# Kernel optimization log

Measured on AMD Instinct MI355X. Metric: run time of the kernel, lower is better.

Reference implementation:

```python
import jax, jax.numpy as jnp
import numpy as np

EPS = 1e-5

def _temporal_conv(x_bcnt, w, b):
    # x: (B,C,N,T), w: (O,I,1,K), pad time dim by K//2
    k = w.shape[-1]
    y = jax.lax.conv_general_dilated(
        x_bcnt, w, window_strides=(1, 1),
        padding=[(0, 0), (k // 2, k // 2)],
        dimension_numbers=("NCHW", "OIHW", "NCHW"))
    return y + b[None, :, None, None]

def _gcn(x_btnc, edge_index, w, b):
    # GCNConv: add self-loops, symmetric normalization, linear, scatter-add, bias.
    B, T, N, C = x_btnc.shape
    src = jnp.concatenate([edge_index[0], jnp.arange(N)])
    dst = jnp.concatenate([edge_index[1], jnp.arange(N)])
    ew = jnp.ones(src.shape[0], dtype=x_btnc.dtype)
    deg = jax.ops.segment_sum(ew, dst, num_segments=N)
    dinv = jnp.where(deg > 0, jax.lax.rsqrt(jnp.maximum(deg, 1e-12)), 0.0)
    norm = dinv[src] * dinv[dst] * ew  # (E+N,)
    xh = jnp.einsum("btnc,cd->btnd", x_btnc, w)
    msgs = xh[:, :, src, :] * norm[None, None, :, None]  # (B,T,E+N,C)
    agg = jnp.zeros_like(xh).at[:, :, dst, :].add(msgs)
    return agg + b

def _batchnorm2d(x_bcnt, gamma, beta):
    mean = jnp.mean(x_bcnt, axis=(0, 2, 3), keepdims=True)
    var = jnp.mean((x_bcnt - mean) ** 2, axis=(0, 2, 3), keepdims=True)
    xn = (x_bcnt - mean) * jax.lax.rsqrt(var + EPS)
    return xn * gamma[None, :, None, None] + beta[None, :, None, None]

def setup_inputs() -> dict:
    key = jax.random.key(0)
    ks = jax.random.split(key, 10)
    B, T, N, C = 1, 64, 2000, 64
    E, K = 32000, 3
    s = 1.0 / np.sqrt(C * K)
    inp = {
        "x": jax.random.normal(ks[0], (B, T, N, C), dtype=jnp.float32),
        "edge_index": jax.random.randint(ks[1], (2, E), 0, N, dtype=jnp.int64),
        "conv1_w": jax.random.uniform(ks[2], (C, C, 1, K), jnp.float32, -s, s),
        "conv1_b": jax.random.uniform(ks[3], (C,), jnp.float32, -s, s),
        "gcn_w": jax.random.normal(ks[4], (C, C), dtype=jnp.float32) / np.sqrt(C),
        "gcn_b": jnp.zeros((C,), dtype=jnp.float32),
        "conv2_w": jax.random.uniform(ks[5], (C, C, 1, K), jnp.float32, -s, s),
        "conv2_b": jax.random.uniform(ks[6], (C,), jnp.float32, -s, s),
        "bn_gamma": jnp.ones((C,), dtype=jnp.float32),
        "bn_beta": jnp.zeros((C,), dtype=jnp.float32),
    }
    return inp

def reference(x, edge_index, conv1_w, conv1_b, gcn_w, gcn_b, conv2_w, conv2_b, bn_gamma, bn_beta):
    # x: (B,T,N,C) -> (B,C,N,T)
    h = jnp.transpose(x, (0, 3, 2, 1))
    h = _temporal_conv(h, conv1_w, conv1_b)
    h = jnp.transpose(h, (0, 3, 2, 1))  # (B,T,N,C)
    h = _gcn(h, edge_index, gcn_w, gcn_b)
    h = jnp.transpose(h, (0, 3, 2, 1))  # (B,C,N,T)
    h = _temporal_conv(h, conv2_w, conv2_b)
    h = _batchnorm2d(h, bn_gamma, bn_beta)
    h = jax.nn.relu(h)
    return jnp.transpose(h, (0, 3, 2, 1))  # (B,T,N,C)
```

## Files before the change

### kernel.cpp

```cpp
#include <hip/hip_runtime.h>

#define T_DIM 64
#define N_DIM 2000
#define C_DIM 64
#define E_DIM 32000
#define ROWS (T_DIM * N_DIM)
#define BN_EPS 1e-5f
#define TCHUNK 4
#define GEMAX 1024

typedef short s8v __attribute__((ext_vector_type(8)));
typedef float f4v __attribute__((ext_vector_type(4)));

__device__ __forceinline__ ushort f2b(float f) {
    unsigned u = __float_as_uint(f);
    unsigned r = u + 0x7FFF + ((u >> 16) & 1);
    return (ushort)(r >> 16);
}
__device__ __forceinline__ float b2f(ushort h) {
    return __uint_as_float(((unsigned)h) << 16);
}
__device__ __forceinline__ s8v pack8(float4 a, float4 b) {
    s8v r;
    r[0] = (short)f2b(a.x); r[1] = (short)f2b(a.y);
    r[2] = (short)f2b(a.z); r[3] = (short)f2b(a.w);
    r[4] = (short)f2b(b.x); r[5] = (short)f2b(b.y);
    r[6] = (short)f2b(b.z); r[7] = (short)f2b(b.w);
    return r;
}

__global__ void k_degscan(const int* __restrict__ ei, int* __restrict__ offs,
                          float* __restrict__ dinv, int* __restrict__ cursor,
                          int2* __restrict__ edat) {
    __shared__ int a[2048], b[2048];
    int tid = threadIdx.x;
    for (int i = tid; i < 2048; i += 1024) a[i] = 0;
    __syncthreads();
    for (int e = tid; e < E_DIM; e += 1024) atomicAdd(&a[ei[E_DIM + e]], 1);
    __syncthreads();
    for (int i = tid; i < 2048; i += 1024) a[i] = (i < N_DIM) ? (a[i] + 1) : 0;
    __syncthreads();
    int* s = a; int* d = b;
    for (int off = 1; off < 2048; off <<= 1) {
        for (int i = tid; i < 2048; i += 1024)
            d[i] = s[i] + ((i >= off) ? s[i - off] : 0);
        __syncthreads();
        int* t = s; s = d; d = t;
    }
    for (int i = tid; i < 2048; i += 1024)
        if (i <= N_DIM) offs[i] = (i == 0) ? 0 : s[i - 1];
    for (int n = tid; n < N_DIM; n += 1024) {
        int pre = (n == 0) ? 0 : s[n - 1];
        int dp1 = s[n] - pre;
        float dn = rsqrtf((float)dp1);
        dinv[n] = dn;
        edat[pre] = make_int2(n, __float_as_int(dn * dn));
        cursor[n] = 1;
    }
}

__global__ __launch_bounds__(256) void k_fillw(
    const int* __restrict__ ei, const int* __restrict__ offs,
    const float* __restrict__ dinv, int* __restrict__ cursor,
    int2* __restrict__ edat,
    const float* __restrict__ c1w, const float* __restrict__ c1b,
    const float* __restrict__ gw, const float* __restrict__ gb,
    const float* __restrict__ c2b, const float* __restrict__ c2w,
    ushort* __restrict__ W5f, ushort* __restrict__ Wc,
    float* __restrict__ bz, float* __restrict__ beta) {
    int tid = threadIdx.x;
    if (blockIdx.x < 125) {
        int e = blockIdx.x * 256 + tid;
        if (e < E_DIM) {
            int s = ei[e];
            int d = ei[E_DIM + e];
            int p = atomicAdd(&cursor[d], 1);
            edat[offs[d] + p] = make_int2(s, __float_as_int(dinv[s] * dinv[d]));
        }
        return;
    }
    __shared__ float Gl[3][64];
    __shared__ float b1l[64], gbl[64];
    int i = blockIdx.x - 125;
    if (tid < 192) {
        int j = tid >> 6, c = tid & 63;
        float s = 0.f;
        for (int o = 0; o < 64; ++o)
            s += c1w[o * 192 + i * 3 + j] * gw[o * 64 + c];
        Gl[j][c] = s;
    } else {
        int c = tid - 192;
        float s = 0.f;
        if (i == 0)
            for (int o = 0; o < 64; ++o) s += c1b[o] * gw[o * 64 + c];
        b1l[c] = s;
        gbl[c] = gb[c];
    }
    __syncthreads();
    if (tid < 64) {
        int n = tid;
        float d00 = 0.f, d01 = 0.f, d02 = 0.f;
        float d10 = 0.f, d11 = 0.f, d12 = 0.f;
        float d20 = 0.f, d21 = 0.f, d22 = 0.f;
        for (int c = 0; c < 64; ++c) {
            float a0 = Gl[0][c], a1 = Gl[1][c], a2 = Gl[2][c];
            float b0 = c2w[n * 192 + c * 3 + 0];
            float b1 = c2w[n * 192 + c * 3 + 1];
            float b2 = c2w[n * 192 + c * 3 + 2];
            d00 += a0 * b0; d01 += a0 * b1; d02 += a0 * b2;
            d10 += a1 * b0; d11 += a1 * b1; d12 += a1 * b2;
            d20 += a2 * b0; d21 += a2 * b1; d22 += a2 * b2;
        }
        float wm[5];
        wm[0] = d00;
        wm[1] = d01 + d10;
        wm[2] = d02 + d11 + d20;
        wm[3] = d12 + d21;
        wm[4] = d22;
        for (int m = 0; m < 5; ++m) {
            int kk = m * 64 + i;
            int flat = (((kk >> 5) * 4 + (n >> 4)) * 64 + ((kk >> 3) & 3) * 16 + (n & 15)) * 8 + (kk & 7);
            W5f[flat] = f2b(wm[m]);
        }
        int fc = (((i >> 5) * 4 + (n >> 4)) * 64 + ((i >> 3) & 3) * 16 + (n & 15)) * 8 + (i & 7);
        Wc[fc] = f2b(-d20);
        Wc[4096 + fc] = f2b(-d02);
        if (i == 0) {
            float s1[3] = {0.f, 0.f, 0.f}, s2[3] = {0.f, 0.f, 0.f};
            for (int k = 0; k < 3; ++k)
                for (int c = 0; c < 64; ++c) {
                    float w2 = c2w[n * 192 + c * 3 + k];
                    s1[k] += b1l[c] * w2;
                    s2[k] += gbl[c] * w2;
                }
            bz[n]        = s1[0] + s1[1] + s1[2];
            bz[64 + n]   = s1[1] + s1[2];
            bz[128 + n]  = s1[0] + s1[1];
            float cb = c2b[n];
            beta[n]       = s2[0] + s2[1] + s2[2] + cb;
            beta[64 + n]  = s2[1] + s2[2] + cb;
            beta[128 + n] = s2[0] + s2[1] + cb;
        }
    }
}

__global__ __launch_bounds__(256) void k_conv5(
    const float* __restrict__ x, const ushort* __restrict__ W5f,
    const ushort* __restrict__ Wcg, const float* __restrict__ bz,
    ushort* __restrict__ z) {
    __shared__ __align__(16) ushort Wl[20480];
    __shared__ __align__(16) ushort Cl[4096];
    __shared__ __align__(16) ushort Eb[4][1280];

    int tid = threadIdx.x, wv = tid >> 6, lane = tid & 63;
    int ml = lane & 15, q = lane >> 4;
    int n0 = blockIdx.x * 64;
    int t0 = blockIdx.y * TCHUNK;
    int n = n0 + wv * 16 + ml;
    bool nok = (n < N_DIM);
    const float* xrow = x + (size_t)n * 64 + q * 8;

    #pragma unroll
    for (int o = 0; o < 10; ++o) {
        int idx = tid + o * 256;
        *(s8v*)&Wl[idx * 8] = *(const s8v*)&W5f[idx * 8];
    }
    bool bnd0 = (t0 == 0), bnd1 = (t0 + TCHUNK == T_DIM);
    if (bnd0 || bnd1) {
        const ushort* src = Wcg + (bnd1 ? 4096 : 0);
        #pragma unroll
        for (int o = 0; o < 2; ++o) {
            int idx = tid + o * 256;
            *(s8v*)&Cl[idx * 8] = *(const s8v*)&src[idx * 8];
        }
    }

    const s8v ZV = {0, 0, 0, 0, 0, 0, 0, 0};
    s8v a[16];
    #pragma unroll
    for (int i = 0; i < 16; ++i) a[i] = ZV;

    #pragma unroll
    for (int i = 0; i < 5; ++i) {
        int s = t0 - 2 + i;
        if (nok && s >= 0 && s < T_DIM) {
            const float* p = xrow + (size_t)s * N_DIM * 64;
            float4 v0 = *(const float4*)p;
            float4 v1 = *(const float4*)(p + 4);
            float4 v2 = *(const float4*)(p + 32);
            float4 v3 = *(const float4*)(p + 36);
            a[2 * i]     = pack8(v0, v1);
            a[2 * i + 1] = pack8(v2, v3);
        }
    }
    __syncthreads();

    #pragma unroll
    for (int p = 0; p < TCHUNK; ++p) {
        int t = t0 + p;
        float4 r0, r1, r2, r3;
        bool pf = false;
        if (p < TCHUNK - 1) {
            int s = t0 + 3 + p;
            if (nok && s < T_DIM) {
                pf = true;
                const float* pp = xrow + (size_t)s * N_DIM * 64;
                r0 = *(const float4*)pp;
                r1 = *(const float4*)(pp + 4);
                r2 = *(const float4*)(pp + 32);
                r3 = *(const float4*)(pp + 36);
            }
        }

        f4v acc[4];
        #pragma unroll
        for (int c = 0; c < 4; ++c) acc[c] = (f4v){0.f, 0.f, 0.f, 0.f};

        #pragma unroll
        for (int sg = 0; sg < 10; ++sg) {
            #pragma unroll
            for (int c = 0; c < 4; ++c) {
                s8v bf = *(const s8v*)&Wl[((sg * 4 + c) * 64 + lane) * 8];
                acc[c] = __builtin_amdgcn_mfma_f32_16x16x32_bf16(a[2 * p + sg], bf, acc[c], 0, 0, 0);
            }
        }
        if (bnd0 && p == 0) {
            #pragma unroll
            for (int s2 = 0; s2 < 2; ++s2)
                #pragma unroll
                for (int c = 0; c < 4; ++c) {
                    s8v bf = *(const s8v*)&Cl[((s2 * 4 + c) * 64 + lane) * 8];
                    acc[c] = __builtin_amdgcn_mfma_f32_16x16x32_bf16(a[4 + s2], bf, acc[c], 0, 0, 0);
                }
        }
        if (bnd1 && p == TCHUNK - 1) {
            #pragma unroll
            for (int s2 = 0; s2 < 2; ++s2)
                #pragma unroll
                for (int c = 0; c < 4; ++c) {
                    s8v bf = *(const s8v*)&Cl[((s2 * 4 + c) * 64 + lane) * 8];
                    acc[c] = __builtin_amdgcn_mfma_f32_16x16x32_bf16(a[10 + s2], bf, acc[c], 0, 0, 0);
                }
        }

        int cls = (bnd0 && p == 0) ? 1 : ((bnd1 && p == TCHUNK - 1) ? 2 : 0);
        ushort* eb = &Eb[wv][0];
        #pragma unroll
        for (int c = 0; c < 4; ++c) {
            int col = c * 16 + ml;
            float bb = bz[cls * 64 + col];
            #pragma unroll
            for (int rg = 0; rg < 4; ++rg)
                eb[(q * 4 + rg) * 80 + col] = f2b(acc[c][rg] + bb);
        }
        int rr = lane >> 2, cof = (lane & 3) * 16;
        int gn = n0 + wv * 16 + rr;
        if (gn < N_DIM) {
            ushort* dst = &z[((size_t)t * N_DIM + gn) * 64 + cof];
            *(s8v*)dst       = *(const s8v*)&eb[rr * 80 + cof];
            *(s8v*)(dst + 8) = *(const s8v*)&eb[rr * 80 + cof + 8];
        }
        if (p < TCHUNK - 1) {
            a[10 + 2 * p] = pf ? pack8(r0, r1) : ZV;
            a[11 + 2 * p] = pf ? pack8(r2, r3) : ZV;
        }
    }
}

__global__ __launch_bounds__(512) void k_gather(
    const ushort* __restrict__ zb, const int* __restrict__ offs,
    const int2* __restrict__ edat, const float* __restrict__ beta,
    ushort* __restrict__ yb, float* __restrict__ pstats) {
    __shared__ float ssum[64], ssq[64];
    __shared__ int2 eLds[GEMAX];
    __shared__ int eoff[9];
    int tid = threadIdx.x;
    if (tid < 64) { ssum[tid] = 0.f; ssq[tid] = 0.f; }

    int tg = blockIdx.x;
    int nb = blockIdx.y;
    int n0 = nb * 8;
    if (tid < 9) eoff[tid] = offs[n0 + tid];
    __syncthreads();
    int ebase = eoff[0];
    int ecnt = eoff[8] - ebase;
    bool inLds = (ecnt <= GEMAX);
    if (inLds)
        for (int i = tid; i < ecnt; i += 512) eLds[i] = edat[ebase + i];
    __syncthreads();

    int wv = tid >> 6, lane = tid & 63;
    int u = lane >> 3;
    int c8 = (lane & 7) * 8;
    int t = tg * 8 + u;
    int cls = (t == 0) ? 1 : ((t == 63) ? 2 : 0);
    const float* bp = beta + cls * 64 + c8;
    float4 b0 = *(const float4*)bp;
    float4 b1 = *(const float4*)(bp + 4);
    float bb[8] = {b0.x, b0.y, b0.z, b0.w, b1.x, b1.y, b1.z, b1.w};
    const ushort* zl = zb + (size_t)t * (N_DIM * 64) + c8;

    int n = n0 + wv;
    int beg = eoff[wv] - ebase;
    int len = eoff[wv + 1] - ebase - beg;

    float acc[8] = {0.f,0.f,0.f,0.f,0.f,0.f,0.f,0.f};

    if (inLds) {
        for (int k = 0; k < len; k += 8) {
            int2 e[8];
            #pragma unroll
            for (int i = 0; i < 8; ++i) {
                int kk = k + i;
                e[i] = eLds[beg + (kk < len ? kk : 0)];
            }
            s8v v[8];
            #pragma unroll
            for (int i = 0; i < 8; ++i)
                v[i] = *(const s8v*)(zl + (size_t)e[i].x * 64);
            #pragma unroll
            for (int i = 0; i < 8; ++i) {
                float w = (k + i < len) ? __int_as_float(e[i].y) : 0.f;
                #pragma unroll
                for (int j = 0; j < 8; ++j) acc[j] += w * b2f((ushort)v[i][j]);
            }
        }
    } else {
        const int2* eg = edat + ebase;
        for (int k = 0; k < len; ++k) {
            int2 e = eg[beg + k];
            float w = __int_as_float(e.y);
            s8v v = *(const s8v*)(zl + (size_t)e.x * 64);
            #pragma unroll
            for (int i = 0; i < 8; ++i) acc[i] += w * b2f((ushort)v[i]);
        }
    }

    float sr[8], qr[8];
    s8v pk;
    #pragma unroll
    for (int i = 0; i < 8; ++i) {
        float y = acc[i] + bb[i];
        pk[i] = (short)f2b(y);
        sr[i] = y;
        qr[i] = y * y;
    }
    *(s8v*)&yb[((size_t)t * N_DIM + n) * 64 + c8] = pk;

    #pragma unroll
    for (int dd = 8; dd <= 32; dd <<= 1)
        #pragma unroll
        for (int i = 0; i < 8; ++i) {
            sr[i] += __shfl_xor(sr[i], dd);
            qr[i] += __shfl_xor(qr[i], dd);
        }
    if (u == 0) {
        #pragma unroll
        for (int i = 0; i < 8; ++i) {
            atomicAdd(&ssum[c8 + i], sr[i]);
            atomicAdd(&ssq[c8 + i], qr[i]);
        }
    }
    __syncthreads();
    int b = tg * 250 + nb;
    if (tid < 64) {
        pstats[(size_t)tid * 2000 + b]        = ssum[tid];
        pstats[(size_t)(64 + tid) * 2000 + b] = ssq[tid];
    }
}

__global__ __launch_bounds__(256) void k_red(const float* __restrict__ pstats,
                                             float* __restrict__ bnstats) {
    __shared__ float ws[4];
    int row = blockIdx.x;
    const float* p = pstats + (size_t)row * 2000;
    int tid = threadIdx.x;
    float s = 0.f;
    for (int i = tid; i < 2000; i += 256) s += p[i];
    #pragma unroll
    for (int d = 1; d < 64; d <<= 1) s += __shfl_xor(s, d);
    if ((tid & 63) == 0) ws[tid >> 6] = s;
    __syncthreads();
    if (tid == 0) bnstats[row] = ws[0] + ws[1] + ws[2] + ws[3];
}

__global__ __launch_bounds__(256) void k_bn(const ushort* __restrict__ yb,
                                            const float* __restrict__ bnstats,
                                            const float* __restrict__ gamma,
                                            const float* __restrict__ beta,
                                            float* __restrict__ out) {
    __shared__ float sscale[64], sshift[64];
    int tid = threadIdx.x;
    if (tid < 64) {
        float m = bnstats[tid] * (1.0f / ROWS);
        float v = bnstats[64 + tid] * (1.0f / ROWS) - m * m;
        float sc = gamma[tid] * rsqrtf(v + BN_EPS);
        sscale[tid] = sc;
        sshift[tid] = beta[tid] - m * sc;
    }
    __syncthreads();
    const int total8 = ROWS * 8;
    for (int i8 = blockIdx.x * 256 + tid; i8 < total8; i8 += gridDim.x * 256) {
        s8v v = *(const s8v*)&yb[(size_t)i8 * 8];
        int c8 = (i8 & 7) * 8;
        f4v o0, o1;
        o0[0] = fmaxf(b2f((ushort)v[0]) * sscale[c8 + 0] + sshift[c8 + 0], 0.f);
        o0[1] = fmaxf(b2f((ushort)v[1]) * sscale[c8 + 1] + sshift[c8 + 1], 0.f);
        o0[2] = fmaxf(b2f((ushort)v[2]) * sscale[c8 + 2] + sshift[c8 + 2], 0.f);
        o0[3] = fmaxf(b2f((ushort)v[3]) * sscale[c8 + 3] + sshift[c8 + 3], 0.f);
        o1[0] = fmaxf(b2f((ushort)v[4]) * sscale[c8 + 4] + sshift[c8 + 4], 0.f);
        o1[1] = fmaxf(b2f((ushort)v[5]) * sscale[c8 + 5] + sshift[c8 + 5], 0.f);
        o1[2] = fmaxf(b2f((ushort)v[6]) * sscale[c8 + 6] + sshift[c8 + 6], 0.f);
        o1[3] = fmaxf(b2f((ushort)v[7]) * sscale[c8 + 7] + sshift[c8 + 7], 0.f);
        __builtin_nontemporal_store(o0, (f4v*)&out[(size_t)i8 * 8]);
        __builtin_nontemporal_store(o1, (f4v*)&out[(size_t)i8 * 8 + 4]);
    }
}

extern "C" void kernel_launch(void* const* d_in, const int* in_sizes, int n_in,
                              void* d_out, int out_size, void* d_ws, size_t ws_size,
                              hipStream_t stream) {
    const float* x   = (const float*)d_in[0];
    const int*   ei  = (const int*)d_in[1];
    const float* c1w = (const float*)d_in[2];
    const float* c1b = (const float*)d_in[3];
    const float* gw  = (const float*)d_in[4];
    const float* gb  = (const float*)d_in[5];
    const float* c2w = (const float*)d_in[6];
    const float* c2b = (const float*)d_in[7];
    const float* bng = (const float*)d_in[8];
    const float* bnb = (const float*)d_in[9];
    float* out = (float*)d_out;

    ushort* yb     = (ushort*)d_ws;
    ushort* W5f    = yb + (size_t)ROWS * 64;
    ushort* Wc     = W5f + 20480;
    float*  bz     = (float*)(Wc + 8192);
    float*  beta   = bz + 192;
    float*  dinv   = beta + 192;
    float*  bnstats= dinv + 2000;
    int*    offs   = (int*)(bnstats + 128);
    int*    cursor = offs + 2001;
    int2*   edat   = (int2*)((char*)(cursor + 2000) +
                     (((size_t)(cursor + 2000)) % 8 ? 4 : 0));
    float*  pstats = (float*)(edat + (E_DIM + N_DIM));

    ushort* zb = (ushort*)d_out;

    k_degscan<<<1, 1024, 0, stream>>>(ei, offs, dinv, cursor, edat);
    k_fillw<<<189, 256, 0, stream>>>(ei, offs, dinv, cursor, edat,
                                     c1w, c1b, gw, gb, c2b, c2w, W5f, Wc, bz, beta);
    k_conv5<<<dim3(32, T_DIM / TCHUNK), 256, 0, stream>>>(x, W5f, Wc, bz, zb);
    k_gather<<<dim3(8, 250), 512, 0, stream>>>(zb, offs, edat, beta, yb, pstats);
    k_red<<<128, 256, 0, stream>>>(pstats, bnstats);
    k_bn<<<2048, 256, 0, stream>>>(yb, bnstats, bng, bnb, out);
}
```

Baseline: 180.0 us.

## Fuse gather, BN reduction and BN apply into one cooperative kernel

Replaces the three final launches (gather+partial stats, stats reduction, BN+ReLU apply) with a single cooperative kernel of 512 blocks. Blocks loop over node groups and use grid-wide syncs between phases. This removes two kernel launches and their gaps, at the cost of grid-sync overhead and lower parallelism in the gather phase. It falls back to the old three-kernel path if the cooperative launch fails.

```diff
diff --git a/kernel.cpp b/kernel.cpp
--- a/kernel.cpp
+++ b/kernel.cpp
@@ -1,4 +1,7 @@
 #include <hip/hip_runtime.h>
+#include <hip/hip_cooperative_groups.h>
+
+namespace cg = cooperative_groups;
 
 #define T_DIM 64
 #define N_DIM 2000
@@ -267,6 +270,162 @@
     }
 }
 
+__global__ __launch_bounds__(512, 4) void k_gbn(
+    const ushort* __restrict__ zb, const int* __restrict__ offs,
+    const int2* __restrict__ edat, const float* __restrict__ gbeta,
+    ushort* __restrict__ yb, float* __restrict__ pstats,
+    float* __restrict__ bnstats, const float* __restrict__ gamma,
+    const float* __restrict__ bnb, float* __restrict__ out) {
+    __shared__ float ssum[64], ssq[64];
+    __shared__ int2 eLds[GEMAX];
+    __shared__ int eoff[9];
+    __shared__ float sws[8];
+    __shared__ float sscale[64], sshift[64];
+
+    int tid = threadIdx.x;
+    int tg = blockIdx.x;
+    int nb0 = blockIdx.y;
+    int wv = tid >> 6, lane = tid & 63;
+    int u = lane >> 3;
+    int c8 = (lane & 7) * 8;
+    int t = tg * 8 + u;
+    int cls = (t == 0) ? 1 : ((t == 63) ? 2 : 0);
+    const float* bp = gbeta + cls * 64 + c8;
+    float4 bv0 = *(const float4*)bp;
+    float4 bv1 = *(const float4*)(bp + 4);
+    float bb[8] = {bv0.x, bv0.y, bv0.z, bv0.w, bv1.x, bv1.y, bv1.z, bv1.w};
+    const ushort* zl = zb + (size_t)t * (N_DIM * 64) + c8;
+
+    for (int grp = nb0; grp < 250; grp += 64) {
+        int n0 = grp * 8;
+        if (tid < 64) { ssum[tid] = 0.f; ssq[tid] = 0.f; }
+        if (tid < 9) eoff[tid] = offs[n0 + tid];
+        __syncthreads();
+        int ebase = eoff[0];
+        int ecnt = eoff[8] - ebase;
+        bool inLds = (ecnt <= GEMAX);
+        if (inLds)
+            for (int i = tid; i < ecnt; i += 512) eLds[i] = edat[ebase + i];
+        __syncthreads();
+
+        int n = n0 + wv;
+        int beg = eoff[wv] - ebase;
+        int len = eoff[wv + 1] - ebase - beg;
+
+        float acc[8] = {0.f,0.f,0.f,0.f,0.f,0.f,0.f,0.f};
+        if (inLds) {
+            for (int k = 0; k < len; k += 8) {
+                int2 e[8];
+                #pragma unroll
+                for (int i = 0; i < 8; ++i) {
+                    int kk = k + i;
+                    e[i] = eLds[beg + (kk < len ? kk : 0)];
+                }
+                s8v v[8];
+                #pragma unroll
+                for (int i = 0; i < 8; ++i)
+                    v[i] = *(const s8v*)(zl + (size_t)e[i].x * 64);
+                #pragma unroll
+                for (int i = 0; i < 8; ++i) {
+                    float w = (k + i < len) ? __int_as_float(e[i].y) : 0.f;
+                    #pragma unroll
+                    for (int j = 0; j < 8; ++j) acc[j] += w * b2f((ushort)v[i][j]);
+                }
+            }
+        } else {
+            const int2* eg = edat + ebase;
+            for (int k = 0; k < len; ++k) {
+                int2 e = eg[beg + k];
+                float w = __int_as_float(e.y);
+                s8v v = *(const s8v*)(zl + (size_t)e.x * 64);
+                #pragma unroll
+                for (int i = 0; i < 8; ++i) acc[i] += w * b2f((ushort)v[i]);
+            }
+        }
+
+        float sr[8], qr[8];
+        s8v pk;
+        #pragma unroll
+        for (int i = 0; i < 8; ++i) {
+            float y = acc[i] + bb[i];
+            pk[i] = (short)f2b(y);
+            sr[i] = y;
+            qr[i] = y * y;
+        }
+        *(s8v*)&yb[((size_t)t * N_DIM + n) * 64 + c8] = pk;
+
+        #pragma unroll
+        for (int dd = 8; dd <= 32; dd <<= 1)
+            #pragma unroll
+            for (int i = 0; i < 8; ++i) {
+                sr[i] += __shfl_xor(sr[i], dd);
+                qr[i] += __shfl_xor(qr[i], dd);
+            }
+        if (u == 0) {
+            #pragma unroll
+            for (int i = 0; i < 8; ++i) {
+                atomicAdd(&ssum[c8 + i], sr[i]);
+                atomicAdd(&ssq[c8 + i], qr[i]);
+            }
+        }
+        __syncthreads();
+        int b = tg * 250 + grp;
+        if (tid < 64) {
+            pstats[(size_t)tid * 2000 + b]        = ssum[tid];
+            pstats[(size_t)(64 + tid) * 2000 + b] = ssq[tid];
+        }
+    }
+    __threadfence();
+    cg::this_grid().sync();
+
+    int linb = blockIdx.y * 8 + blockIdx.x;
+    if (linb < 128) {
+        const float* p = pstats + (size_t)linb * 2000;
+        float s = 0.f;
+        for (int i = tid; i < 2000; i += 512) s += p[i];
+        #pragma unroll
+        for (int d = 1; d < 64; d <<= 1) s += __shfl_xor(s, d);
+        if (lane == 0) sws[wv] = s;
+        __syncthreads();
+        if (tid == 0) {
+            float tot = 0.f;
+            #pragma unroll
+            for (int i = 0; i < 8; ++i) tot += sws[i];
+            bnstats[linb] = tot;
+        }
+    }
+    __threadfence();
+    cg::this_grid().sync();
+
+    if (tid < 64) {
+        float m = bnstats[tid] * (1.0f / ROWS);
+        float v = bnstats[64 + tid] * (1.0f / ROWS) - m * m;
+        float sc = gamma[tid] * rsqrtf(v + BN_EPS);
+        sscale[tid] = sc;
+        sshift[tid] = bnb[tid] - m * sc;
+    }
+    __syncthreads();
+    float scl[8], sft[8];
+    #pragma unroll
+    for (int i = 0; i < 8; ++i) { scl[i] = sscale[c8 + i]; sft[i] = sshift[c8 + i]; }
+    for (int grp = nb0; grp < 250; grp += 64) {
+        int n = grp * 8 + wv;
+        size_t base = ((size_t)t * N_DIM + n) * 64 + c8;
+        s8v v = *(const s8v*)&yb[base];
+        f4v o0, o1;
+        o0[0] = fmaxf(b2f((ushort)v[0]) * scl[0] + sft[0], 0.f);
+        o0[1] = fmaxf(b2f((ushort)v[1]) * scl[1] + sft[1], 0.f);
+        o0[2] = fmaxf(b2f((ushort)v[2]) * scl[2] + sft[2], 0.f);
+        o0[3] = fmaxf(b2f((ushort)v[3]) * scl[3] + sft[3], 0.f);
+        o1[0] = fmaxf(b2f((ushort)v[4]) * scl[4] + sft[4], 0.f);
+        o1[1] = fmaxf(b2f((ushort)v[5]) * scl[5] + sft[5], 0.f);
+        o1[2] = fmaxf(b2f((ushort)v[6]) * scl[6] + sft[6], 0.f);
+        o1[3] = fmaxf(b2f((ushort)v[7]) * scl[7] + sft[7], 0.f);
+        __builtin_nontemporal_store(o0, (f4v*)&out[base]);
+        __builtin_nontemporal_store(o1, (f4v*)&out[base + 4]);
+    }
+}
+
 __global__ __launch_bounds__(512) void k_gather(
     const ushort* __restrict__ zb, const int* __restrict__ offs,
     const int2* __restrict__ edat, const float* __restrict__ beta,
@@ -305,7 +464,6 @@
     int len = eoff[wv + 1] - ebase - beg;
 
     float acc[8] = {0.f,0.f,0.f,0.f,0.f,0.f,0.f,0.f};
-
     if (inLds) {
         for (int k = 0; k < len; k += 8) {
             int2 e[8];
@@ -451,7 +609,19 @@
     k_fillw<<<189, 256, 0, stream>>>(ei, offs, dinv, cursor, edat,
                                      c1w, c1b, gw, gb, c2b, c2w, W5f, Wc, bz, beta);
     k_conv5<<<dim3(32, T_DIM / TCHUNK), 256, 0, stream>>>(x, W5f, Wc, bz, zb);
-    k_gather<<<dim3(8, 250), 512, 0, stream>>>(zb, offs, edat, beta, yb, pstats);
-    k_red<<<128, 256, 0, stream>>>(pstats, bnstats);
-    k_bn<<<2048, 256, 0, stream>>>(yb, bnstats, bng, bnb, out);
-}
+
+    const ushort* zb_c = zb;
+    const int* offs_c = offs;
+    const int2* edat_c = edat;
+    const float* beta_c = beta;
+    void* kargs[] = {(void*)&zb_c, (void*)&offs_c, (void*)&edat_c, (void*)&beta_c,
+                     (void*)&yb, (void*)&pstats, (void*)&bnstats,
+                     (void*)&bng, (void*)&bnb, (void*)&out};
+    hipError_t err = hipLaunchCooperativeKernel((void*)k_gbn, dim3(8, 64), dim3(512),
+                                                kargs, 0, stream);
+    if (err != hipSuccess) {
+        k_gather<<<dim3(8, 250), 512, 0, stream>>>(zb, offs, edat, beta, yb, pstats);
+        k_red<<<128, 256, 0, stream>>>(pstats, bnstats);
+        k_bn<<<2048, 256, 0, stream>>>(yb, bnstats, bng, bnb, out);
+    }
+}
```

New measurement: 478.9 us. 166% more time.
